# Kernel tuning notes

Measured on AMD Instinct MI355X. Metric: run time of the kernel, lower is better.

The kernel has to match this reference:

```python
import jax, jax.numpy as jnp
import numpy as np

NF, NM, E = 100000, 20000, 1000000
H, FIN, MIN = 128, 8, 5


def setup_inputs() -> dict:
    key = jax.random.key(0)
    ks = jax.random.split(key, 32)

    def w(k, out_d, in_d):
        return jax.random.normal(k, (out_d, in_d), jnp.float32) / np.sqrt(in_d).astype(np.float32)

    inp = {}
    inp["x_fund"] = jax.random.normal(ks[0], (NF, FIN), jnp.float32)
    inp["x_manager"] = jax.random.normal(ks[1], (NM, MIN), jnp.float32)
    inp["fm_src"] = jax.random.randint(ks[2], (E,), 0, NF, jnp.int32)
    inp["fm_dst"] = jax.random.randint(ks[3], (E,), 0, NM, jnp.int32)
    # input projections
    inp["Wf"] = w(ks[4], H, FIN); inp["bf"] = jnp.zeros((H,), jnp.float32)
    inp["Wm"] = w(ks[5], H, MIN); inp["bm"] = jnp.zeros((H,), jnp.float32)
    # SAGEConv params per layer/relation: lin_l (neighbor, with bias), lin_r (root, no bias)
    i = 6
    for l in range(2):
        for rel in ("fm", "mf"):
            inp[f"Wl_{rel}{l}"] = w(ks[i], H, H); i += 1
            inp[f"bl_{rel}{l}"] = jnp.zeros((H,), jnp.float32)
            inp[f"Wr_{rel}{l}"] = w(ks[i], H, H); i += 1
    # classifier MLP (dropout is identity at inference)
    inp["Wc1"] = w(ks[i], H // 2, H); inp["bc1"] = jnp.zeros((H // 2,), jnp.float32); i += 1
    inp["Wc2"] = w(ks[i], 2, H // 2); inp["bc2"] = jnp.zeros((2,), jnp.float32)
    return inp


def _sage(x_src, x_dst, src, dst, Wl, bl, Wr, n_dst):
    # SAGEConv: lin_l(mean_{j in N(i)} x_j) + lin_r(x_i); mean of empty set -> 0
    msg = x_src[src]  # [E, H] gather
    agg = jax.ops.segment_sum(msg, dst, num_segments=n_dst)
    deg = jax.ops.segment_sum(jnp.ones_like(dst, dtype=x_src.dtype), dst, num_segments=n_dst)
    mean = agg / jnp.maximum(deg, 1.0)[:, None]
    return mean @ Wl.T + bl + x_dst @ Wr.T


def reference(x_fund, x_manager, fm_src, fm_dst, Wf, bf, Wm, bm,
              Wl_fm0, bl_fm0, Wr_fm0, Wl_mf0, bl_mf0, Wr_mf0,
              Wl_fm1, bl_fm1, Wr_fm1, Wl_mf1, bl_mf1, Wr_mf1,
              Wc1, bc1, Wc2, bc2):
    f = jax.nn.relu(x_fund @ Wf.T + bf)       # [NF, H]
    m = jax.nn.relu(x_manager @ Wm.T + bm)    # [NM, H]
    # layer 0: fund->manager and manager->fund (rev = transposed edges)
    m1 = jax.nn.relu(_sage(f, m, fm_src, fm_dst, Wl_fm0, bl_fm0, Wr_fm0, NM))
    f1 = jax.nn.relu(_sage(m, f, fm_dst, fm_src, Wl_mf0, bl_mf0, Wr_mf0, NF))
    # layer 1
    m2 = jax.nn.relu(_sage(f1, m1, fm_src, fm_dst, Wl_fm1, bl_fm1, Wr_fm1, NM))
    f2 = jax.nn.relu(_sage(m1, f1, fm_dst, fm_src, Wl_mf1, bl_mf1, Wr_mf1, NF))
    del m2
    # classifier on fund nodes (dropout=eval identity)
    h = jax.nn.relu(f2 @ Wc1.T + bc1)
    return h @ Wc2.T + bc2  # [NF, 2]
```

## Files before the change

kernel.cpp:

```cpp
#include <hip/hip_runtime.h>
#include <hip/hip_bf16.h>

#define HDIM 128
#define NG 8
#define NB 32

typedef unsigned short u16;
typedef unsigned int u32;
typedef __attribute__((ext_vector_type(8))) short bf16x8;
typedef __attribute__((ext_vector_type(4))) float f32x4;

__device__ __forceinline__ float bf2f(u16 u) {
  union { u32 i; float f; } x; x.i = ((u32)u) << 16; return x.f;
}
__device__ __forceinline__ u16 f2bf(float f) {
  union { float f; u32 i; } x; x.f = f;
  u32 r = x.i + 0x7fffu + ((x.i >> 16) & 1u);
  return (u16)(r >> 16);
}

static __device__ __forceinline__ int dmin(int a, int b) { return a < b ? a : b; }

__global__ __launch_bounds__(1024) void k_hist2(const int* __restrict__ src, const int* __restrict__ dst,
                                                int* __restrict__ cnt, int E, int NF, int NM) {
  __shared__ int h[15104];
  int g = blockIdx.x & (NG - 1);
  int c = blockIdx.x >> 3;
  int t = threadIdx.x;
  int NFg = (NF + NG - 1) / NG, NMg = (NM + NG - 1) / NG;
  int loF = g * NFg, hiF = dmin(NF, loF + NFg);
  int loM = g * NMg, hiM = dmin(NM, loM + NMg);
  int nb = NFg + NMg;
  for (int j = t; j < nb; j += 1024) h[j] = 0;
  __syncthreads();
  int Epc = (E + NB - 1) / NB;
  int c0 = c * Epc, c1 = dmin(E, c0 + Epc);
  for (int i = c0 + t; i < c1; i += 1024) {
    int s = src[i], d = dst[i];
    if (s >= loF && s < hiF) atomicAdd(&h[s - loF], 1);
    if (d >= loM && d < hiM) atomicAdd(&h[NFg + (d - loM)], 1);
  }
  __syncthreads();
  size_t K = (size_t)NF + NM;
  int* cc = cnt + (size_t)c * K;
  for (int j = t; j < NFg; j += 1024) {
    int k = loF + j;
    if (k < hiF) cc[k] = h[j];
  }
  for (int j = t; j < NMg; j += 1024) {
    int k = loM + j;
    if (k < hiM) cc[NF + k] = h[NFg + j];
  }
}

__global__ __launch_bounds__(256) void k_colscan(int* __restrict__ cnt, int* __restrict__ deg, int K) {
  int k = blockIdx.x * 256 + threadIdx.x;
  if (k >= K) return;
  int s = 0;
  #pragma unroll 4
  for (int c = 0; c < NB; ++c) {
    int* p = cnt + (size_t)c * K + k;
    int v = *p;
    *p = s;
    s += v;
  }
  deg[k] = s;
}

__global__ __launch_bounds__(256) void k_scan_chunks2(const int* __restrict__ deg, int NF, int NM,
                                                      int nchf, int* __restrict__ rp_f, int* __restrict__ rp_m,
                                                      int* __restrict__ part_f, int* __restrict__ part_m) {
  __shared__ int sm[256];
  int t = threadIdx.x;
  bool isM = (int)blockIdx.x >= nchf;
  int b = isM ? (blockIdx.x - nchf) : blockIdx.x;
  const int* d = isM ? (deg + NF) : deg;
  int n = isM ? NM : NF;
  int* rowptr = isM ? rp_m : rp_f;
  int* part = isM ? part_m : part_f;
  int base = b * 1024 + t * 4;
  int v0 = 0, v1 = 0, v2 = 0, v3 = 0;
  if (base + 0 < n) v0 = d[base + 0];
  if (base + 1 < n) v1 = d[base + 1];
  if (base + 2 < n) v2 = d[base + 2];
  if (base + 3 < n) v3 = d[base + 3];
  int s = v0 + v1 + v2 + v3;
  sm[t] = s;
  __syncthreads();
  for (int off = 1; off < 256; off <<= 1) {
    int x = (t >= off) ? sm[t - off] : 0;
    __syncthreads();
    sm[t] += x;
    __syncthreads();
  }
  int excl = sm[t] - s;
  if (t == 255) part[b] = sm[255];
  if (base + 0 < n) rowptr[base + 0] = excl;
  if (base + 1 < n) rowptr[base + 1] = excl + v0;
  if (base + 2 < n) rowptr[base + 2] = excl + v0 + v1;
  if (base + 3 < n) rowptr[base + 3] = excl + v0 + v1 + v2;
}

__global__ __launch_bounds__(256) void k_scan_part2(int* __restrict__ part_f, int nchf,
                                                    int* __restrict__ part_m, int nchm) {
  __shared__ int sm[256];
  int t = threadIdx.x;
  int* part = blockIdx.x ? part_m : part_f;
  int nb = blockIdx.x ? nchm : nchf;
  int s = (t < nb) ? part[t] : 0;
  sm[t] = s;
  __syncthreads();
  for (int off = 1; off < 256; off <<= 1) {
    int x = (t >= off) ? sm[t - off] : 0;
    __syncthreads();
    sm[t] += x;
    __syncthreads();
  }
  if (t < nb) part[t] = sm[t] - s;
}

__global__ __launch_bounds__(256) void k_add_off2(int* __restrict__ rp_f, const int* __restrict__ part_f, int NF,
                                                  int* __restrict__ rp_m, const int* __restrict__ part_m, int NM,
                                                  int total) {
  int i = blockIdx.x * 256 + threadIdx.x;
  int s = gridDim.x * 256;
  int tot = NF + NM;
  for (; i < tot; i += s) {
    if (i < NF) rp_f[i] += part_f[i >> 10];
    else { int j = i - NF; rp_m[j] += part_m[j >> 10]; }
  }
  if (blockIdx.x == 0 && threadIdx.x == 0) { rp_f[NF] = total; rp_m[NM] = total; }
}

__global__ __launch_bounds__(1024) void k_scatter2(const int* __restrict__ src, const int* __restrict__ dst,
                                                   const int* __restrict__ rp_f, const int* __restrict__ rp_m,
                                                   const int* __restrict__ cnt,
                                                   int* __restrict__ col_f, int* __restrict__ col_m,
                                                   int E, int NF, int NM) {
  __shared__ int cur[15104];
  int g = blockIdx.x & (NG - 1);
  int c = blockIdx.x >> 3;
  int t = threadIdx.x;
  int NFg = (NF + NG - 1) / NG, NMg = (NM + NG - 1) / NG;
  int loF = g * NFg, hiF = dmin(NF, loF + NFg);
  int loM = g * NMg, hiM = dmin(NM, loM + NMg);
  size_t K = (size_t)NF + NM;
  const int* cc = cnt + (size_t)c * K;
  for (int j = t; j < NFg; j += 1024) {
    int k = loF + j;
    if (k < hiF) cur[j] = rp_f[k] + cc[k];
  }
  for (int j = t; j < NMg; j += 1024) {
    int k = loM + j;
    if (k < hiM) cur[NFg + j] = rp_m[k] + cc[NF + k];
  }
  __syncthreads();
  int Epc = (E + NB - 1) / NB;
  int c0 = c * Epc, c1 = dmin(E, c0 + Epc);
  for (int i = c0 + t; i < c1; i += 1024) {
    int s = src[i], d = dst[i];
    if (s >= loF && s < hiF) {
      int p = atomicAdd(&cur[s - loF], 1);
      col_f[p] = d;
    }
    if (d >= loM && d < hiM) {
      int p = atomicAdd(&cur[NFg + (d - loM)], 1);
      col_m[p] = s;
    }
  }
}

__global__ __launch_bounds__(256) void k_w2bf(const float* __restrict__ s0, const float* __restrict__ s1,
                                              const float* __restrict__ s2, const float* __restrict__ s3,
                                              const float* __restrict__ s4, const float* __restrict__ s5,
                                              const float* __restrict__ s6, u16* __restrict__ dst) {
  int i = blockIdx.x * 256 + threadIdx.x;
  const float* s; int off = i;
  if (i < 16384) { s = s0; }
  else if (i < 32768) { s = s1; off = i - 16384; }
  else if (i < 49152) { s = s2; off = i - 32768; }
  else if (i < 65536) { s = s3; off = i - 49152; }
  else if (i < 81920) { s = s4; off = i - 65536; }
  else if (i < 98304) { s = s5; off = i - 81920; }
  else { s = s6; off = i - 98304; }
  dst[i] = f2bf(s[off]);
}

__global__ __launch_bounds__(256) void k_proj2(const float* __restrict__ xf, const float* __restrict__ Wf,
                                               const float* __restrict__ bfp, const float* __restrict__ xm,
                                               const float* __restrict__ Wm, const float* __restrict__ bmp,
                                               u16* __restrict__ outf, u16* __restrict__ outm,
                                               int NF, int NM) {
  __shared__ float Wfs[128 * 9];
  __shared__ float Wms[128 * 5];
  __shared__ float bsf[128];
  __shared__ float bsm[128];
  int t = threadIdx.x;
  for (int i = t; i < 128 * 8; i += 256) {
    int c = i >> 3, k = i & 7;
    Wfs[c * 9 + k] = Wf[i];
  }
  for (int i = t; i < 128 * 5; i += 256) {
    int c = i / 5, k = i - c * 5;
    Wms[c * 5 + k] = Wm[i];
  }
  for (int i = t; i < 128; i += 256) { bsf[i] = bfp[i]; bsm[i] = bmp[i]; }
  __syncthreads();
  int totF = NF * 64;
  int tot = totF + NM * 64;
  int idx = blockIdx.x * 256 + t;
  int gs = gridDim.x * 256;
  for (; idx < tot; idx += gs) {
    if (idx < totF) {
      int row = idx >> 6, cp = (idx & 63) * 2;
      float a0 = bsf[cp], a1 = bsf[cp + 1];
      const float* xr = xf + (size_t)row * 8;
      #pragma unroll
      for (int k = 0; k < 8; ++k) {
        float xv = xr[k];
        a0 += Wfs[cp * 9 + k] * xv;
        a1 += Wfs[(cp + 1) * 9 + k] * xv;
      }
      a0 = fmaxf(a0, 0.f); a1 = fmaxf(a1, 0.f);
      u32 pk = (u32)f2bf(a0) | ((u32)f2bf(a1) << 16);
      *(u32*)(outf + (size_t)row * HDIM + cp) = pk;
    } else {
      int k2 = idx - totF;
      int row = k2 >> 6, cp = (k2 & 63) * 2;
      float a0 = bsm[cp], a1 = bsm[cp + 1];
      const float* xr = xm + (size_t)row * 5;
      #pragma unroll
      for (int k = 0; k < 5; ++k) {
        float xv = xr[k];
        a0 += Wms[cp * 5 + k] * xv;
        a1 += Wms[(cp + 1) * 5 + k] * xv;
      }
      a0 = fmaxf(a0, 0.f); a1 = fmaxf(a1, 0.f);
      u32 pk = (u32)f2bf(a0) | ((u32)f2bf(a1) << 16);
      *(u32*)(outm + (size_t)row * HDIM + cp) = pk;
    }
  }
}

__global__ __launch_bounds__(256) void k_agg2(const u16* __restrict__ feat, const int* __restrict__ rowptr,
                                              const int* __restrict__ col, u16* __restrict__ out, int ndst) {
  int t = threadIdx.x;
  int grp = t >> 4, lc = t & 15;
  int nd = blockIdx.x * 16 + grp;
  if (nd >= ndst) return;
  int s0 = rowptr[nd], s1 = rowptr[nd + 1];
  float a0=0.f,a1=0.f,a2=0.f,a3=0.f,a4=0.f,a5=0.f,a6=0.f,a7=0.f;
  const u16* fb = feat + lc * 8;
  int j = s0;
  for (; j + 3 < s1; j += 4) {
    uint4 v0 = *(const uint4*)(fb + (size_t)col[j]     * HDIM);
    uint4 v1 = *(const uint4*)(fb + (size_t)col[j + 1] * HDIM);
    uint4 v2 = *(const uint4*)(fb + (size_t)col[j + 2] * HDIM);
    uint4 v3 = *(const uint4*)(fb + (size_t)col[j + 3] * HDIM);
    a0 += bf2f((u16)v0.x) + bf2f((u16)v1.x) + bf2f((u16)v2.x) + bf2f((u16)v3.x);
    a1 += bf2f((u16)(v0.x>>16)) + bf2f((u16)(v1.x>>16)) + bf2f((u16)(v2.x>>16)) + bf2f((u16)(v3.x>>16));
    a2 += bf2f((u16)v0.y) + bf2f((u16)v1.y) + bf2f((u16)v2.y) + bf2f((u16)v3.y);
    a3 += bf2f((u16)(v0.y>>16)) + bf2f((u16)(v1.y>>16)) + bf2f((u16)(v2.y>>16)) + bf2f((u16)(v3.y>>16));
    a4 += bf2f((u16)v0.z) + bf2f((u16)v1.z) + bf2f((u16)v2.z) + bf2f((u16)v3.z);
    a5 += bf2f((u16)(v0.z>>16)) + bf2f((u16)(v1.z>>16)) + bf2f((u16)(v2.z>>16)) + bf2f((u16)(v3.z>>16));
    a6 += bf2f((u16)v0.w) + bf2f((u16)v1.w) + bf2f((u16)v2.w) + bf2f((u16)v3.w);
    a7 += bf2f((u16)(v0.w>>16)) + bf2f((u16)(v1.w>>16)) + bf2f((u16)(v2.w>>16)) + bf2f((u16)(v3.w>>16));
  }
  for (; j < s1; ++j) {
    uint4 v = *(const uint4*)(fb + (size_t)col[j] * HDIM);
    a0 += bf2f((u16)v.x); a1 += bf2f((u16)(v.x >> 16));
    a2 += bf2f((u16)v.y); a3 += bf2f((u16)(v.y >> 16));
    a4 += bf2f((u16)v.z); a5 += bf2f((u16)(v.z >> 16));
    a6 += bf2f((u16)v.w); a7 += bf2f((u16)(v.w >> 16));
  }
  float inv = (s1 > s0) ? 1.f / (float)(s1 - s0) : 0.f;
  uint4 pk;
  pk.x = (u32)f2bf(a0 * inv) | ((u32)f2bf(a1 * inv) << 16);
  pk.y = (u32)f2bf(a2 * inv) | ((u32)f2bf(a3 * inv) << 16);
  pk.z = (u32)f2bf(a4 * inv) | ((u32)f2bf(a5 * inv) << 16);
  pk.w = (u32)f2bf(a6 * inv) | ((u32)f2bf(a7 * inv) << 16);
  *(uint4*)(out + (size_t)nd * HDIM + lc * 8) = pk;
}

__global__ __launch_bounds__(256) void k_aggd(const u16* __restrict__ tc, const int* __restrict__ rowptr,
                                              const int* __restrict__ col, u16* __restrict__ aggc, int ndst) {
  int t = threadIdx.x;
  int grp = t >> 5, lc = t & 31;
  int nd = blockIdx.x * 8 + grp;
  if (nd >= ndst) return;
  int s0 = rowptr[nd], s1 = rowptr[nd + 1];
  float a0=0.f,a1=0.f,a2=0.f,a3=0.f,a4=0.f,a5=0.f,a6=0.f,a7=0.f;
  const u16* fb = tc + lc * 8;
  int j = s0;
  for (; j + 3 < s1; j += 4) {
    uint4 v0 = *(const uint4*)(fb + (size_t)col[j]     * 256);
    uint4 v1 = *(const uint4*)(fb + (size_t)col[j + 1] * 256);
    uint4 v2 = *(const uint4*)(fb + (size_t)col[j + 2] * 256);
    uint4 v3 = *(const uint4*)(fb + (size_t)col[j + 3] * 256);
    a0 += bf2f((u16)v0.x) + bf2f((u16)v1.x) + bf2f((u16)v2.x) + bf2f((u16)v3.x);
    a1 += bf2f((u16)(v0.x>>16)) + bf2f((u16)(v1.x>>16)) + bf2f((u16)(v2.x>>16)) + bf2f((u16)(v3.x>>16));
    a2 += bf2f((u16)v0.y) + bf2f((u16)v1.y) + bf2f((u16)v2.y) + bf2f((u16)v3.y);
    a3 += bf2f((u16)(v0.y>>16)) + bf2f((u16)(v1.y>>16)) + bf2f((u16)(v2.y>>16)) + bf2f((u16)(v3.y>>16));
    a4 += bf2f((u16)v0.z) + bf2f((u16)v1.z) + bf2f((u16)v2.z) + bf2f((u16)v3.z);
    a5 += bf2f((u16)(v0.z>>16)) + bf2f((u16)(v1.z>>16)) + bf2f((u16)(v2.z>>16)) + bf2f((u16)(v3.z>>16));
    a6 += bf2f((u16)v0.w) + bf2f((u16)v1.w) + bf2f((u16)v2.w) + bf2f((u16)v3.w);
    a7 += bf2f((u16)(v0.w>>16)) + bf2f((u16)(v1.w>>16)) + bf2f((u16)(v2.w>>16)) + bf2f((u16)(v3.w>>16));
  }
  for (; j < s1; ++j) {
    uint4 v = *(const uint4*)(fb + (size_t)col[j] * 256);
    a0 += bf2f((u16)v.x); a1 += bf2f((u16)(v.x >> 16));
    a2 += bf2f((u16)v.y); a3 += bf2f((u16)(v.y >> 16));
    a4 += bf2f((u16)v.z); a5 += bf2f((u16)(v.z >> 16));
    a6 += bf2f((u16)v.w); a7 += bf2f((u16)(v.w >> 16));
  }
  float inv = (s1 > s0) ? 1.f / (float)(s1 - s0) : 0.f;
  uint4 pk;
  pk.x = (u32)f2bf(a0 * inv) | ((u32)f2bf(a1 * inv) << 16);
  pk.y = (u32)f2bf(a2 * inv) | ((u32)f2bf(a3 * inv) << 16);
  pk.z = (u32)f2bf(a4 * inv) | ((u32)f2bf(a5 * inv) << 16);
  pk.w = (u32)f2bf(a6 * inv) | ((u32)f2bf(a7 * inv) << 16);
  *(uint4*)(aggc + (size_t)nd * 256 + lc * 8) = pk;
}

__global__ __launch_bounds__(256) void k_ling(const u16* __restrict__ X1, const u16* __restrict__ W1,
                                              const u16* __restrict__ X2, const u16* __restrict__ W2,
                                              const u16* __restrict__ ADD, const float* __restrict__ bias,
                                              u16* __restrict__ out, int n, int do_relu,
                                              int ostride, int astride) {
  int t = threadIdx.x;
  int w = t >> 6, lane = t & 63;
  int lm = lane & 15, lk = (lane >> 4) * 8;
  int cg = (lane >> 4) * 4;
  int row0 = blockIdx.x * 128 + w * 32;
  if (row0 >= n) return;
  int r0 = row0 + lm;       if (r0 >= n) r0 = n - 1;
  int r1 = row0 + 16 + lm;  if (r1 >= n) r1 = n - 1;
  f32x4 acc0[8], acc1[8];
  #pragma unroll
  for (int i = 0; i < 8; ++i) { acc0[i] = (f32x4){0.f,0.f,0.f,0.f}; acc1[i] = (f32x4){0.f,0.f,0.f,0.f}; }
  const u16* Xp = X1;
  const u16* Wp = W1;
  for (int p = 0; p < 2; ++p) {
    #pragma unroll
    for (int ks = 0; ks < 4; ++ks) {
      bf16x8 b0 = *(const bf16x8*)(Xp + (size_t)r0 * 128 + ks * 32 + lk);
      bf16x8 b1 = *(const bf16x8*)(Xp + (size_t)r1 * 128 + ks * 32 + lk);
      #pragma unroll
      for (int nt = 0; nt < 8; ++nt) {
        bf16x8 a = *(const bf16x8*)(Wp + (size_t)(nt * 16 + lm) * 128 + ks * 32 + lk);
        acc0[nt] = __builtin_amdgcn_mfma_f32_16x16x32_bf16(a, b0, acc0[nt], 0, 0, 0);
        acc1[nt] = __builtin_amdgcn_mfma_f32_16x16x32_bf16(a, b1, acc1[nt], 0, 0, 0);
      }
    }
    if (!X2) break;
    Xp = X2;
    Wp = W2;
  }
  #pragma unroll
  for (int half = 0; half < 2; ++half) {
    int m = row0 + half * 16 + lm;
    if (m >= n) break;
    f32x4* acc = half ? acc1 : acc0;
    #pragma unroll
    for (int nt = 0; nt < 8; ++nt) {
      int c = nt * 16 + cg;
      float v0 = acc[nt][0], v1 = acc[nt][1], v2 = acc[nt][2], v3 = acc[nt][3];
      if (bias) {
        float4 bv = *(const float4*)(bias + c);
        v0 += bv.x; v1 += bv.y; v2 += bv.z; v3 += bv.w;
      }
      if (ADD) {
        ushort4 av = *(const ushort4*)(ADD + (size_t)m * astride + c);
        v0 += bf2f(av.x); v1 += bf2f(av.y); v2 += bf2f(av.z); v3 += bf2f(av.w);
      }
      if (do_relu) {
        v0 = fmaxf(v0, 0.f); v1 = fmaxf(v1, 0.f); v2 = fmaxf(v2, 0.f); v3 = fmaxf(v3, 0.f);
      }
      ushort4 pk;
      pk.x = f2bf(v0); pk.y = f2bf(v1); pk.z = f2bf(v2); pk.w = f2bf(v3);
      *(ushort4*)(out + (size_t)m * ostride + c) = pk;
    }
  }
}

__global__ __launch_bounds__(256) void k_ling2(const u16* __restrict__ XA, const u16* __restrict__ WA,
                                               const u16* __restrict__ XB, const u16* __restrict__ WB,
                                               u16* __restrict__ out, int n) {
  int nb = gridDim.x >> 1;
  bool second = (int)blockIdx.x >= nb;
  const u16* X = second ? XB : XA;
  const u16* W = second ? WB : WA;
  int bid = second ? (blockIdx.x - nb) : blockIdx.x;
  u16* o = out + (second ? 128 : 0);
  int t = threadIdx.x;
  int w = t >> 6, lane = t & 63;
  int lm = lane & 15, lk = (lane >> 4) * 8;
  int cg = (lane >> 4) * 4;
  int row0 = bid * 128 + w * 32;
  if (row0 >= n) return;
  int r0 = row0 + lm;       if (r0 >= n) r0 = n - 1;
  int r1 = row0 + 16 + lm;  if (r1 >= n) r1 = n - 1;
  f32x4 acc0[8], acc1[8];
  #pragma unroll
  for (int i = 0; i < 8; ++i) { acc0[i] = (f32x4){0.f,0.f,0.f,0.f}; acc1[i] = (f32x4){0.f,0.f,0.f,0.f}; }
  #pragma unroll
  for (int ks = 0; ks < 4; ++ks) {
    bf16x8 b0 = *(const bf16x8*)(X + (size_t)r0 * 128 + ks * 32 + lk);
    bf16x8 b1 = *(const bf16x8*)(X + (size_t)r1 * 128 + ks * 32 + lk);
    #pragma unroll
    for (int nt = 0; nt < 8; ++nt) {
      bf16x8 a = *(const bf16x8*)(W + (size_t)(nt * 16 + lm) * 128 + ks * 32 + lk);
      acc0[nt] = __builtin_amdgcn_mfma_f32_16x16x32_bf16(a, b0, acc0[nt], 0, 0, 0);
      acc1[nt] = __builtin_amdgcn_mfma_f32_16x16x32_bf16(a, b1, acc1[nt], 0, 0, 0);
    }
  }
  #pragma unroll
  for (int half = 0; half < 2; ++half) {
    int m = row0 + half * 16 + lm;
    if (m >= n) break;
    f32x4* acc = half ? acc1 : acc0;
    #pragma unroll
    for (int nt = 0; nt < 8; ++nt) {
      int c = nt * 16 + cg;
      ushort4 pk;
      pk.x = f2bf(acc[nt][0]); pk.y = f2bf(acc[nt][1]);
      pk.z = f2bf(acc[nt][2]); pk.w = f2bf(acc[nt][3]);
      *(ushort4*)(o + (size_t)m * 256 + c) = pk;
    }
  }
}

__global__ __launch_bounds__(256) void k_cls(const u16* __restrict__ f2, const u16* __restrict__ Wc1bf,
                                             const float* __restrict__ bc1, const float* __restrict__ Wc2,
                                             const float* __restrict__ bc2, float* __restrict__ out, int n) {
  int t = threadIdx.x;
  int w = t >> 6, lane = t & 63;
  int lm = lane & 15, lk = (lane >> 4) * 8;
  int cg = (lane >> 4) * 4;
  int row0 = blockIdx.x * 64 + w * 16;
  if (row0 >= n) return;
  int rB = row0 + lm;
  if (rB >= n) rB = n - 1;
  f32x4 acc[4];
  #pragma unroll
  for (int i = 0; i < 4; ++i) acc[i] = (f32x4){0.f, 0.f, 0.f, 0.f};
  #pragma unroll
  for (int ks = 0; ks < 4; ++ks) {
    bf16x8 b = *(const bf16x8*)(f2 + (size_t)rB * 128 + ks * 32 + lk);
    #pragma unroll
    for (int nt = 0; nt < 4; ++nt) {
      bf16x8 a = *(const bf16x8*)(Wc1bf + (size_t)(nt * 16 + lm) * 128 + ks * 32 + lk);
      acc[nt] = __builtin_amdgcn_mfma_f32_16x16x32_bf16(a, b, acc[nt], 0, 0, 0);
    }
  }
  float s0 = 0.f, s1 = 0.f;
  #pragma unroll
  for (int nt = 0; nt < 4; ++nt) {
    int k = nt * 16 + cg;
    float4 bv = *(const float4*)(bc1 + k);
    float4 w0 = *(const float4*)(Wc2 + k);
    float4 w1 = *(const float4*)(Wc2 + 64 + k);
    float h0 = fmaxf(acc[nt][0] + bv.x, 0.f);
    float h1 = fmaxf(acc[nt][1] + bv.y, 0.f);
    float h2 = fmaxf(acc[nt][2] + bv.z, 0.f);
    float h3 = fmaxf(acc[nt][3] + bv.w, 0.f);
    s0 += h0 * w0.x + h1 * w0.y + h2 * w0.z + h3 * w0.w;
    s1 += h0 * w1.x + h1 * w1.y + h2 * w1.z + h3 * w1.w;
  }
  s0 += __shfl_xor(s0, 16); s1 += __shfl_xor(s1, 16);
  s0 += __shfl_xor(s0, 32); s1 += __shfl_xor(s1, 32);
  int m = row0 + lm;
  if (lane < 16 && m < n) {
    out[(size_t)m * 2 + 0] = s0 + bc2[0];
    out[(size_t)m * 2 + 1] = s1 + bc2[1];
  }
}

static inline int imin(int a, int b) { return a < b ? a : b; }

extern "C" void kernel_launch(void* const* d_in, const int* in_sizes, int n_in,
                              void* d_out, int out_size, void* d_ws, size_t ws_size,
                              hipStream_t stream) {
  const float* x_fund = (const float*)d_in[0];
  const float* x_mgr  = (const float*)d_in[1];
  const int* fm_src   = (const int*)d_in[2];
  const int* fm_dst   = (const int*)d_in[3];
  const float* Wf = (const float*)d_in[4];
  const float* bfb = (const float*)d_in[5];
  const float* Wm = (const float*)d_in[6];
  const float* bm = (const float*)d_in[7];
  const float* Wl_fm0 = (const float*)d_in[8];
  const float* bl_fm0 = (const float*)d_in[9];
  const float* Wr_fm0 = (const float*)d_in[10];
  const float* Wl_mf0 = (const float*)d_in[11];
  const float* bl_mf0 = (const float*)d_in[12];
  const float* Wr_mf0 = (const float*)d_in[13];
  const float* Wl_mf1 = (const float*)d_in[17];
  const float* bl_mf1 = (const float*)d_in[18];
  const float* Wr_mf1 = (const float*)d_in[19];
  const float* Wc1 = (const float*)d_in[20];
  const float* bc1 = (const float*)d_in[21];
  const float* Wc2 = (const float*)d_in[22];
  const float* bc2 = (const float*)d_in[23];

  int NF = in_sizes[0] / 8;
  int NM = in_sizes[1] / 5;
  int E  = in_sizes[2];
  int K  = NF + NM;

  char* ws = (char*)d_ws;
  size_t off = 0;
  auto alloc = [&](size_t bytes) -> char* {
    char* p = ws + off;
    off += (bytes + 255) & ~(size_t)255;
    return p;
  };
  u16* f_b   = (u16*)alloc((size_t)NF * HDIM * 2);
  u16* f1_b  = (u16*)alloc((size_t)NF * HDIM * 2);
  u16* f2_b  = (u16*)alloc((size_t)NF * HDIM * 2);
  u16* aggc  = (u16*)alloc((size_t)NF * 256 * 2);
  u16* m_b   = (u16*)alloc((size_t)NM * HDIM * 2);
  u16* m1_b  = (u16*)alloc((size_t)NM * HDIM * 2);
  u16* tcomb = (u16*)alloc((size_t)NM * 256 * 2);
  u16* aggm  = (u16*)alloc((size_t)NM * HDIM * 2);
  u16* wbf   = (u16*)alloc((size_t)106496 * 2);
  int* rp_f  = (int*)alloc((size_t)(NF + 1) * 4);
  int* rp_m  = (int*)alloc((size_t)(NM + 1) * 4);
  int* deg   = (int*)alloc((size_t)K * 4);
  int* col_f = (int*)alloc((size_t)E * 4);
  int* col_m = (int*)alloc((size_t)E * 4);
  int* cnt   = (int*)alloc((size_t)NB * K * 4);
  int* part_f = (int*)alloc(256 * 4);
  int* part_m = (int*)alloc(256 * 4);
  (void)ws_size; (void)n_in; (void)out_size;

  u16* Wlfm0b = wbf + 0;
  u16* Wrfm0b = wbf + 16384;
  u16* Wlmf0b = wbf + 32768;
  u16* Wrmf0b = wbf + 49152;
  u16* Wlmf1b = wbf + 65536;
  u16* Wrmf1b = wbf + 81920;
  u16* Wc1b   = wbf + 98304;

  int nch_f = (NF + 1023) / 1024;
  int nch_m = (NM + 1023) / 1024;

  k_w2bf<<<416, 256, 0, stream>>>(Wl_fm0, Wr_fm0, Wl_mf0, Wr_mf0, Wl_mf1, Wr_mf1, Wc1, wbf);

  k_hist2<<<NG * NB, 1024, 0, stream>>>(fm_src, fm_dst, cnt, E, NF, NM);
  k_colscan<<<(K + 255) / 256, 256, 0, stream>>>(cnt, deg, K);
  k_scan_chunks2<<<nch_f + nch_m, 256, 0, stream>>>(deg, NF, NM, nch_f, rp_f, rp_m, part_f, part_m);
  k_scan_part2<<<2, 256, 0, stream>>>(part_f, nch_f, part_m, nch_m);
  k_add_off2<<<(K + 255) / 256, 256, 0, stream>>>(rp_f, part_f, NF, rp_m, part_m, NM, E);
  k_scatter2<<<NG * NB, 1024, 0, stream>>>(fm_src, fm_dst, rp_f, rp_m, cnt, col_f, col_m, E, NF, NM);

  k_proj2<<<imin(((NF + NM) * 64 + 255) / 256, 4096), 256, 0, stream>>>(
      x_fund, Wf, bfb, x_mgr, Wm, bm, f_b, m_b, NF, NM);

  k_agg2<<<(NM + 15) / 16, 256, 0, stream>>>(f_b, rp_m, col_m, aggm, NM);
  k_ling<<<(NM + 127) / 128, 256, 0, stream>>>(aggm, Wlfm0b, m_b, Wrfm0b, nullptr, bl_fm0,
                                               m1_b, NM, 1, 128, 128);

  k_ling2<<<2 * ((NM + 127) / 128), 256, 0, stream>>>(m_b, Wlmf0b, m1_b, Wlmf1b, tcomb, NM);

  k_aggd<<<(NF + 7) / 8, 256, 0, stream>>>(tcomb, rp_f, col_f, aggc, NF);

  k_ling<<<(NF + 127) / 128, 256, 0, stream>>>(f_b, Wrmf0b, nullptr, nullptr, aggc, bl_mf0,
                                               f1_b, NF, 1, 128, 256);
  k_ling<<<(NF + 127) / 128, 256, 0, stream>>>(f1_b, Wrmf1b, nullptr, nullptr, aggc + 128, bl_mf1,
                                               f2_b, NF, 1, 128, 256);

  k_cls<<<(NF + 63) / 64, 256, 0, stream>>>(f2_b, Wc1b, bc1, Wc2, bc2, (float*)d_out, NF);
}
```

Baseline: 307.9 us.

## Fuse column scan into chunk scan, merge weight cast into projection, phase aggd gathers

Merges the per-bucket column scan into the chunked row-pointer scan using vectorized int4 loads, which removes one kernel and the deg buffer. Folds the weight bf16 conversion into the projection kernel to save a launch. Reworks the fund-side aggregation to stash neighbor indices in shared memory and sweep the source rows in 8 index-range phases, so concurrent gathers hit a smaller working set in cache. The phased loop rescans the stash 8 times and serializes the gathers, which trades memory-level parallelism for locality.

```diff
diff --git a/kernel.cpp b/kernel.cpp
--- a/kernel.cpp
+++ b/kernel.cpp
@@ -4,6 +4,8 @@
 #define HDIM 128
 #define NG 8
 #define NB 32
+#define NPH 8
+#define CAP 64
 
 typedef unsigned short u16;
 typedef unsigned int u32;
@@ -53,42 +55,50 @@
   }
 }
 
-__global__ __launch_bounds__(256) void k_colscan(int* __restrict__ cnt, int* __restrict__ deg, int K) {
-  int k = blockIdx.x * 256 + threadIdx.x;
-  if (k >= K) return;
-  int s = 0;
-  #pragma unroll 4
-  for (int c = 0; c < NB; ++c) {
-    int* p = cnt + (size_t)c * K + k;
-    int v = *p;
-    *p = s;
-    s += v;
-  }
-  deg[k] = s;
-}
-
-__global__ __launch_bounds__(256) void k_scan_chunks2(const int* __restrict__ deg, int NF, int NM,
-                                                      int nchf, int* __restrict__ rp_f, int* __restrict__ rp_m,
+__global__ __launch_bounds__(256) void k_scan_chunks3(int* __restrict__ cnt, int NF, int NM, int nchf,
+                                                      int* __restrict__ rp_f, int* __restrict__ rp_m,
                                                       int* __restrict__ part_f, int* __restrict__ part_m) {
   __shared__ int sm[256];
+  int K = NF + NM;
   int t = threadIdx.x;
   bool isM = (int)blockIdx.x >= nchf;
   int b = isM ? (blockIdx.x - nchf) : blockIdx.x;
-  const int* d = isM ? (deg + NF) : deg;
+  int off = isM ? NF : 0;
   int n = isM ? NM : NF;
   int* rowptr = isM ? rp_m : rp_f;
   int* part = isM ? part_m : part_f;
   int base = b * 1024 + t * 4;
   int v0 = 0, v1 = 0, v2 = 0, v3 = 0;
-  if (base + 0 < n) v0 = d[base + 0];
-  if (base + 1 < n) v1 = d[base + 1];
-  if (base + 2 < n) v2 = d[base + 2];
-  if (base + 3 < n) v3 = d[base + 3];
+  if (base + 3 < n && (((off + base) & 3) == 0) && ((K & 3) == 0)) {
+    int s0 = 0, s1 = 0, s2 = 0, s3 = 0;
+    int* p0 = cnt + off + base;
+    #pragma unroll 4
+    for (int c = 0; c < NB; ++c) {
+      int4* p = (int4*)(p0 + (size_t)c * K);
+      int4 x = *p;
+      *p = make_int4(s0, s1, s2, s3);
+      s0 += x.x; s1 += x.y; s2 += x.z; s3 += x.w;
+    }
+    v0 = s0; v1 = s1; v2 = s2; v3 = s3;
+  } else {
+    #pragma unroll
+    for (int i = 0; i < 4; ++i) {
+      int kl = base + i;
+      int s = 0;
+      if (kl < n) {
+        for (int c = 0; c < NB; ++c) {
+          int* p = cnt + (size_t)c * K + off + kl;
+          int x = *p; *p = s; s += x;
+        }
+      }
+      if (i == 0) v0 = s; else if (i == 1) v1 = s; else if (i == 2) v2 = s; else v3 = s;
+    }
+  }
   int s = v0 + v1 + v2 + v3;
   sm[t] = s;
   __syncthreads();
-  for (int off = 1; off < 256; off <<= 1) {
-    int x = (t >= off) ? sm[t - off] : 0;
+  for (int off2 = 1; off2 < 256; off2 <<= 1) {
+    int x = (t >= off2) ? sm[t - off2] : 0;
     __syncthreads();
     sm[t] += x;
     __syncthreads();
@@ -170,27 +180,15 @@
   }
 }
 
-__global__ __launch_bounds__(256) void k_w2bf(const float* __restrict__ s0, const float* __restrict__ s1,
-                                              const float* __restrict__ s2, const float* __restrict__ s3,
-                                              const float* __restrict__ s4, const float* __restrict__ s5,
-                                              const float* __restrict__ s6, u16* __restrict__ dst) {
-  int i = blockIdx.x * 256 + threadIdx.x;
-  const float* s; int off = i;
-  if (i < 16384) { s = s0; }
-  else if (i < 32768) { s = s1; off = i - 16384; }
-  else if (i < 49152) { s = s2; off = i - 32768; }
-  else if (i < 65536) { s = s3; off = i - 49152; }
-  else if (i < 81920) { s = s4; off = i - 65536; }
-  else if (i < 98304) { s = s5; off = i - 81920; }
-  else { s = s6; off = i - 98304; }
-  dst[i] = f2bf(s[off]);
-}
-
-__global__ __launch_bounds__(256) void k_proj2(const float* __restrict__ xf, const float* __restrict__ Wf,
+__global__ __launch_bounds__(256) void k_projw(const float* __restrict__ xf, const float* __restrict__ Wf,
                                                const float* __restrict__ bfp, const float* __restrict__ xm,
                                                const float* __restrict__ Wm, const float* __restrict__ bmp,
                                                u16* __restrict__ outf, u16* __restrict__ outm,
-                                               int NF, int NM) {
+                                               int NF, int NM,
+                                               const float* __restrict__ s0, const float* __restrict__ s1,
+                                               const float* __restrict__ s2, const float* __restrict__ s3,
+                                               const float* __restrict__ s4, const float* __restrict__ s5,
+                                               const float* __restrict__ s6, u16* __restrict__ wdst) {
   __shared__ float Wfs[128 * 9];
   __shared__ float Wms[128 * 5];
   __shared__ float bsf[128];
@@ -206,13 +204,26 @@
   }
   for (int i = t; i < 128; i += 256) { bsf[i] = bfp[i]; bsm[i] = bmp[i]; }
   __syncthreads();
+  const int W2N = 106496;
   int totF = NF * 64;
-  int tot = totF + NM * 64;
+  int tot = W2N + totF + NM * 64;
   int idx = blockIdx.x * 256 + t;
   int gs = gridDim.x * 256;
   for (; idx < tot; idx += gs) {
-    if (idx < totF) {
-      int row = idx >> 6, cp = (idx & 63) * 2;
+    if (idx < W2N) {
+      int i = idx;
+      const float* s; int off = i;
+      if (i < 16384) { s = s0; }
+      else if (i < 32768) { s = s1; off = i - 16384; }
+      else if (i < 49152) { s = s2; off = i - 32768; }
+      else if (i < 65536) { s = s3; off = i - 49152; }
+      else if (i < 81920) { s = s4; off = i - 65536; }
+      else if (i < 98304) { s = s5; off = i - 81920; }
+      else { s = s6; off = i - 98304; }
+      wdst[i] = f2bf(s[off]);
+    } else if (idx < W2N + totF) {
+      int k2 = idx - W2N;
+      int row = k2 >> 6, cp = (k2 & 63) * 2;
       float a0 = bsf[cp], a1 = bsf[cp + 1];
       const float* xr = xf + (size_t)row * 8;
       #pragma unroll
@@ -225,7 +236,7 @@
       u32 pk = (u32)f2bf(a0) | ((u32)f2bf(a1) << 16);
       *(u32*)(outf + (size_t)row * HDIM + cp) = pk;
     } else {
-      int k2 = idx - totF;
+      int k2 = idx - W2N - totF;
       int row = k2 >> 6, cp = (k2 & 63) * 2;
       float a0 = bsm[cp], a1 = bsm[cp + 1];
       const float* xr = xm + (size_t)row * 5;
@@ -283,37 +294,41 @@
 }
 
 __global__ __launch_bounds__(256) void k_aggd(const u16* __restrict__ tc, const int* __restrict__ rowptr,
-                                              const int* __restrict__ col, u16* __restrict__ aggc, int ndst) {
+                                              const int* __restrict__ col, u16* __restrict__ aggc,
+                                              int ndst, int NM) {
+  __shared__ int stash[8][CAP];
   int t = threadIdx.x;
   int grp = t >> 5, lc = t & 31;
   int nd = blockIdx.x * 8 + grp;
   if (nd >= ndst) return;
   int s0 = rowptr[nd], s1 = rowptr[nd + 1];
+  int deg = s1 - s0;
+  int nc = dmin(deg, CAP);
+  for (int jj = lc; jj < nc; jj += 32) stash[grp][jj] = col[s0 + jj];
   float a0=0.f,a1=0.f,a2=0.f,a3=0.f,a4=0.f,a5=0.f,a6=0.f,a7=0.f;
   const u16* fb = tc + lc * 8;
-  int j = s0;
-  for (; j + 3 < s1; j += 4) {
-    uint4 v0 = *(const uint4*)(fb + (size_t)col[j]     * 256);
-    uint4 v1 = *(const uint4*)(fb + (size_t)col[j + 1] * 256);
-    uint4 v2 = *(const uint4*)(fb + (size_t)col[j + 2] * 256);
-    uint4 v3 = *(const uint4*)(fb + (size_t)col[j + 3] * 256);
-    a0 += bf2f((u16)v0.x) + bf2f((u16)v1.x) + bf2f((u16)v2.x) + bf2f((u16)v3.x);
-    a1 += bf2f((u16)(v0.x>>16)) + bf2f((u16)(v1.x>>16)) + bf2f((u16)(v2.x>>16)) + bf2f((u16)(v3.x>>16));
-    a2 += bf2f((u16)v0.y) + bf2f((u16)v1.y) + bf2f((u16)v2.y) + bf2f((u16)v3.y);
-    a3 += bf2f((u16)(v0.y>>16)) + bf2f((u16)(v1.y>>16)) + bf2f((u16)(v2.y>>16)) + bf2f((u16)(v3.y>>16));
-    a4 += bf2f((u16)v0.z) + bf2f((u16)v1.z) + bf2f((u16)v2.z) + bf2f((u16)v3.z);
-    a5 += bf2f((u16)(v0.z>>16)) + bf2f((u16)(v1.z>>16)) + bf2f((u16)(v2.z>>16)) + bf2f((u16)(v3.z>>16));
-    a6 += bf2f((u16)v0.w) + bf2f((u16)v1.w) + bf2f((u16)v2.w) + bf2f((u16)v3.w);
-    a7 += bf2f((u16)(v0.w>>16)) + bf2f((u16)(v1.w>>16)) + bf2f((u16)(v2.w>>16)) + bf2f((u16)(v3.w>>16));
-  }
-  for (; j < s1; ++j) {
+  for (int ph = 0; ph < NPH; ++ph) {
+    int lo = (int)(((long long)NM * ph) / NPH);
+    int hi = (int)(((long long)NM * (ph + 1)) / NPH);
+    for (int j = 0; j < nc; ++j) {
+      int k = stash[grp][j];
+      if (k >= lo && k < hi) {
+        uint4 v = *(const uint4*)(fb + (size_t)k * 256);
+        a0 += bf2f((u16)v.x); a1 += bf2f((u16)(v.x >> 16));
+        a2 += bf2f((u16)v.y); a3 += bf2f((u16)(v.y >> 16));
+        a4 += bf2f((u16)v.z); a5 += bf2f((u16)(v.z >> 16));
+        a6 += bf2f((u16)v.w); a7 += bf2f((u16)(v.w >> 16));
+      }
+    }
+  }
+  for (int j = s0 + nc; j < s1; ++j) {
     uint4 v = *(const uint4*)(fb + (size_t)col[j] * 256);
     a0 += bf2f((u16)v.x); a1 += bf2f((u16)(v.x >> 16));
     a2 += bf2f((u16)v.y); a3 += bf2f((u16)(v.y >> 16));
     a4 += bf2f((u16)v.z); a5 += bf2f((u16)(v.z >> 16));
     a6 += bf2f((u16)v.w); a7 += bf2f((u16)(v.w >> 16));
   }
-  float inv = (s1 > s0) ? 1.f / (float)(s1 - s0) : 0.f;
+  float inv = (deg > 0) ? 1.f / (float)deg : 0.f;
   uint4 pk;
   pk.x = (u32)f2bf(a0 * inv) | ((u32)f2bf(a1 * inv) << 16);
   pk.y = (u32)f2bf(a2 * inv) | ((u32)f2bf(a3 * inv) << 16);
@@ -526,7 +541,6 @@
   u16* wbf   = (u16*)alloc((size_t)106496 * 2);
   int* rp_f  = (int*)alloc((size_t)(NF + 1) * 4);
   int* rp_m  = (int*)alloc((size_t)(NM + 1) * 4);
-  int* deg   = (int*)alloc((size_t)K * 4);
   int* col_f = (int*)alloc((size_t)E * 4);
   int* col_m = (int*)alloc((size_t)E * 4);
   int* cnt   = (int*)alloc((size_t)NB * K * 4);
@@ -545,17 +559,14 @@
   int nch_f = (NF + 1023) / 1024;
   int nch_m = (NM + 1023) / 1024;
 
-  k_w2bf<<<416, 256, 0, stream>>>(Wl_fm0, Wr_fm0, Wl_mf0, Wr_mf0, Wl_mf1, Wr_mf1, Wc1, wbf);
-
   k_hist2<<<NG * NB, 1024, 0, stream>>>(fm_src, fm_dst, cnt, E, NF, NM);
-  k_colscan<<<(K + 255) / 256, 256, 0, stream>>>(cnt, deg, K);
-  k_scan_chunks2<<<nch_f + nch_m, 256, 0, stream>>>(deg, NF, NM, nch_f, rp_f, rp_m, part_f, part_m);
+  k_scan_chunks3<<<nch_f + nch_m, 256, 0, stream>>>(cnt, NF, NM, nch_f, rp_f, rp_m, part_f, part_m);
   k_scan_part2<<<2, 256, 0, stream>>>(part_f, nch_f, part_m, nch_m);
   k_add_off2<<<(K + 255) / 256, 256, 0, stream>>>(rp_f, part_f, NF, rp_m, part_m, NM, E);
   k_scatter2<<<NG * NB, 1024, 0, stream>>>(fm_src, fm_dst, rp_f, rp_m, cnt, col_f, col_m, E, NF, NM);
 
-  k_proj2<<<imin(((NF + NM) * 64 + 255) / 256, 4096), 256, 0, stream>>>(
-      x_fund, Wf, bfb, x_mgr, Wm, bm, f_b, m_b, NF, NM);
+  k_projw<<<4096, 256, 0, stream>>>(x_fund, Wf, bfb, x_mgr, Wm, bm, f_b, m_b, NF, NM,
+                                    Wl_fm0, Wr_fm0, Wl_mf0, Wr_mf0, Wl_mf1, Wr_mf1, Wc1, wbf);
 
   k_agg2<<<(NM + 15) / 16, 256, 0, stream>>>(f_b, rp_m, col_m, aggm, NM);
   k_ling<<<(NM + 127) / 128, 256, 0, stream>>>(aggm, Wlfm0b, m_b, Wrfm0b, nullptr, bl_fm0,
@@ -563,7 +574,7 @@
 
   k_ling2<<<2 * ((NM + 127) / 128), 256, 0, stream>>>(m_b, Wlmf0b, m1_b, Wlmf1b, tcomb, NM);
 
-  k_aggd<<<(NF + 7) / 8, 256, 0, stream>>>(tcomb, rp_f, col_f, aggc, NF);
+  k_aggd<<<(NF + 7) / 8, 256, 0, stream>>>(tcomb, rp_f, col_f, aggc, NF, NM);
 
   k_ling<<<(NF + 127) / 128, 256, 0, stream>>>(f_b, Wrmf0b, nullptr, nullptr, aggc, bl_mf0,
                                                f1_b, NF, 1, 128, 256);
```

New measurement: 362.9 us. 17.9% more time.
